# Optimization experiments

Hardware: AMD Instinct MI355X
Metric: run time of the kernel (lower is better)

Reference implementation:

```python
import jax, jax.numpy as jnp
import numpy as np
from jax import lax

T, B, I, H, FC, O = 2048, 64, 128, 128, 32, 2

def _xavier(key, shape):
    # torch xavier_normal_ on [..., fan_out, fan_in]
    std = float(np.sqrt(2.0 / (shape[-2] + shape[-1])))
    return jax.random.normal(key, shape, jnp.float32) * std

def setup_inputs() -> dict:
    key = jax.random.key(0)
    ks = jax.random.split(key, 16)
    inp = {
        'x': jax.random.normal(ks[0], (T, B, I), jnp.float32),
        'w_ig': _xavier(ks[1], (B, H, I)),
        'w_ii': _xavier(ks[2], (B, H, I)),
        'w_if': _xavier(ks[3], (B, H, I)),
        'w_io': _xavier(ks[4], (B, H, I)),
        'w_hg': _xavier(ks[5], (B, H, H)),
        'w_hi': _xavier(ks[6], (B, H, H)),
        'w_hf': _xavier(ks[7], (B, H, H)),
        'w_ho': _xavier(ks[8], (B, H, H)),
        'b_g': jnp.zeros((B, H, 1), jnp.float32),
        'b_i': jnp.zeros((B, H, 1), jnp.float32),
        'b_f': jnp.zeros((B, H, 1), jnp.float32),
        'b_o': jnp.zeros((B, H, 1), jnp.float32),
        'fc1_w': _xavier(ks[9], (FC, H)),
        'fc1_b': jnp.zeros((FC,), jnp.float32),
        'fc2_w': _xavier(ks[10], (O, FC)),
        'fc2_b': jnp.zeros((O,), jnp.float32),
    }
    return inp

def reference(x, w_ig, w_ii, w_if, w_io, w_hg, w_hi, w_hf, w_ho,
              b_g, b_i, b_f, b_o, fc1_w, fc1_b, fc2_w, fc2_b):
    b, h = w_hg.shape[0], w_hg.shape[1]
    # Original bug: gates read self.hidd which is never updated -> stays zeros.
    hidd0 = jnp.zeros((b, h), x.dtype)
    # Recurrent contributions (identically zero, kept for faithfulness)
    rg = jnp.einsum('bhk,bk->bh', w_hg, hidd0)
    ri = jnp.einsum('bhk,bk->bh', w_hi, hidd0)
    rf = jnp.einsum('bhk,bk->bh', w_hf, hidd0)
    ro = jnp.einsum('bhk,bk->bh', w_ho, hidd0)
    # Input gate pre-activations for all timesteps in one einsum each: [T,B,H]
    g = jnp.tanh(jnp.einsum('bhi,tbi->tbh', w_ig, x) + rg + b_g[:, :, 0])
    i_ = jax.nn.sigmoid(jnp.einsum('bhi,tbi->tbh', w_ii, x) + ri + b_i[:, :, 0])
    f = jax.nn.sigmoid(jnp.einsum('bhi,tbi->tbh', w_if, x) + rf + b_f[:, :, 0])
    o = jax.nn.sigmoid(jnp.einsum('bhi,tbi->tbh', w_io, x) + ro + b_o[:, :, 0])

    def step(carry, gifo):
        c, _ = carry
        g_t, i_t, f_t, o_t = gifo
        c = f_t * c + i_t * g_t
        hid = o_t * jnp.tanh(c)
        return (c, hid), None

    c0 = jnp.zeros((b, h), x.dtype)
    (c_fin, h_fin), _ = lax.scan(step, (c0, c0), (g, i_, f, o))
    # classifier on last hidden: Linear -> tanh -> Linear -> log_softmax
    z = jnp.tanh(h_fin @ fc1_w.T + fc1_b) @ fc2_w.T + fc2_b
    return jax.nn.log_softmax(z, axis=1)
```

## Files before the change

kernel.cpp:

```cpp
#include <hip/hip_runtime.h>
#include <hip/hip_bf16.h>
#include <cstddef>

#define T_DIM 2048
#define B_DIM 64
#define I_DIM 128
#define H_DIM 128
#define FC_DIM 32
#define O_DIM 2

#define NC 16
#define TC (T_DIM / NC)
#define MT 8

#define LOG2E  1.44269504088896f
#define LOG2E2 2.88539008177793f

typedef __attribute__((ext_vector_type(8))) short bf16x8;
typedef __attribute__((ext_vector_type(4))) float f32x4;

__device__ __forceinline__ bf16x8 cvt8(const float* __restrict__ p) {
    union { bf16x8 v; __hip_bfloat162 h2[4]; } u;
#pragma unroll
    for (int j = 0; j < 4; ++j) {
        float2 f2 = {p[2 * j], p[2 * j + 1]};
        u.h2[j] = __float22bfloat162_rn(f2);
    }
    return u.v;
}

__global__ void convert_w_kernel(const float* __restrict__ wg,
                                 const float* __restrict__ wi,
                                 const float* __restrict__ wf,
                                 short* __restrict__ og,
                                 short* __restrict__ oi,
                                 short* __restrict__ of)
{
    const float* src = (blockIdx.y == 0) ? wg : (blockIdx.y == 1) ? wi : wf;
    short* dst       = (blockIdx.y == 0) ? og : (blockIdx.y == 1) ? oi : of;
    const float scale = (blockIdx.y == 0) ? LOG2E2 : LOG2E;
    const size_t idx = ((size_t)blockIdx.x * 256 + threadIdx.x) * 8;
    float4 u0 = *(const float4*)(src + idx);
    float4 u1 = *(const float4*)(src + idx + 4);
    float a[8] = {u0.x * scale, u0.y * scale, u0.z * scale, u0.w * scale,
                  u1.x * scale, u1.y * scale, u1.z * scale, u1.w * scale};
    *(bf16x8*)(dst + idx) = cvt8(a);
}

__global__ __launch_bounds__(512, 4)
void gates_scan_kernel(const float* __restrict__ x,
    const short* __restrict__ wg, const short* __restrict__ wi,
    const short* __restrict__ wf,
    const float* __restrict__ b_g, const float* __restrict__ b_i,
    const float* __restrict__ b_f,
    float* __restrict__ wsF, float* __restrict__ wsA)
{
    __shared__ short frag[MT * 4 * 64 * 8];

    const int L    = threadIdx.x & 63;
    const int wv   = threadIdx.x >> 6;
    const int col  = L & 15;
    const int quad = L >> 4;
    const int bid  = blockIdx.x;
    const int b     = bid & (B_DIM - 1);
    const int chunk = bid >> 6;

    const int h = wv * 16 + col;
    bf16x8 Bg[4], Bi[4], Bf[4];
    {
        const size_t wo = ((size_t)b * H_DIM + h) * I_DIM + quad * 8;
#pragma unroll
        for (int kk = 0; kk < 4; ++kk) {
            Bg[kk] = *(const bf16x8*)(wg + wo + kk * 32);
            Bi[kk] = *(const bf16x8*)(wi + wo + kk * 32);
            Bf[kk] = *(const bf16x8*)(wf + wo + kk * 32);
        }
    }
    const float biasg = b_g[b * H_DIM + h] * LOG2E2;
    const float biasi = b_i[b * H_DIM + h] * LOG2E;
    const float biasf = b_f[b * H_DIM + h] * LOG2E;

    {
        const int mt = wv;
        const int tl = (col >> 2) * 32 + mt * 4 + (col & 3);
        const float* xp = x + ((size_t)(chunk * TC + tl) * B_DIM + b) * I_DIM;
#pragma unroll
        for (int kk = 0; kk < 4; ++kk) {
            const int i0 = quad * 8 + kk * 32;
            float4 u0 = *(const float4*)(xp + i0);
            float4 u1 = *(const float4*)(xp + i0 + 4);
            float a[8] = {u0.x, u0.y, u0.z, u0.w, u1.x, u1.y, u1.z, u1.w};
            *(bf16x8*)(frag + (((mt * 4 + kk) * 64) + L) * 8) = cvt8(a);
        }
    }
    __syncthreads();

    float Fq = 1.0f, Aq = 0.0f;
#pragma unroll 2
    for (int mt = 0; mt < MT; ++mt) {
        bf16x8 ah[4];
#pragma unroll
        for (int kk = 0; kk < 4; ++kk)
            ah[kk] = *(const bf16x8*)(frag + (((mt * 4 + kk) * 64) + L) * 8);
        f32x4 accg = {0.f, 0.f, 0.f, 0.f};
        f32x4 acci = {0.f, 0.f, 0.f, 0.f};
        f32x4 accf = {0.f, 0.f, 0.f, 0.f};
#pragma unroll
        for (int kk = 0; kk < 4; ++kk) {
            accg = __builtin_amdgcn_mfma_f32_16x16x32_bf16(ah[kk], Bg[kk], accg, 0, 0, 0);
            acci = __builtin_amdgcn_mfma_f32_16x16x32_bf16(ah[kk], Bi[kk], acci, 0, 0, 0);
            accf = __builtin_amdgcn_mfma_f32_16x16x32_bf16(ah[kk], Bf[kk], accf, 0, 0, 0);
        }
#pragma unroll
        for (int r = 0; r < 4; ++r) {
            float g  = 2.0f * __builtin_amdgcn_rcpf(
                           1.0f + __builtin_amdgcn_exp2f(-(accg[r] + biasg))) - 1.0f;
            float iv = __builtin_amdgcn_rcpf(
                           1.0f + __builtin_amdgcn_exp2f(-(acci[r] + biasi)));
            float fv = __builtin_amdgcn_rcpf(
                           1.0f + __builtin_amdgcn_exp2f(-(accf[r] + biasf)));
            Aq = fv * Aq + iv * g;
            Fq = fv * Fq;
        }
    }

    float Fo = __shfl_xor(Fq, 16, 64);
    float Ao = __shfl_xor(Aq, 16, 64);
    if ((quad & 1) == 0) { Aq = Fo * Aq + Ao; Fq = Fo * Fq; }
    else                 { Aq = Fq * Ao + Aq; Fq = Fq * Fo; }
    Fo = __shfl_xor(Fq, 32, 64);
    Ao = __shfl_xor(Aq, 32, 64);
    if (quad < 2) { Aq = Fo * Aq + Ao; Fq = Fo * Fq; }
    else          { Aq = Fq * Ao + Aq; Fq = Fq * Fo; }

    if (quad == 0) {
        const int idx = (b * NC + chunk) * H_DIM + h;
        wsF[idx] = Fq;
        wsA[idx] = Aq;
    }
}

__global__ void finish_kernel(const float* __restrict__ x,
    const float* __restrict__ w_io, const float* __restrict__ b_o,
    const float* __restrict__ fc1_w, const float* __restrict__ fc1_b,
    const float* __restrict__ fc2_w, const float* __restrict__ fc2_b,
    const float* __restrict__ wsF, const float* __restrict__ wsA,
    float* __restrict__ out)
{
    const int b = blockIdx.x;
    const int h = threadIdx.x;
    __shared__ float hf[H_DIM];
    __shared__ float z1[FC_DIM];

    float c = 0.0f;
#pragma unroll
    for (int nc = 0; nc < NC; ++nc) {
        const int idx = (b * NC + nc) * H_DIM + h;
        c = wsF[idx] * c + wsA[idx];
    }
    const float* xl = x + ((size_t)(T_DIM - 1) * B_DIM + b) * I_DIM;
    const float* wo = w_io + ((size_t)b * H_DIM + h) * I_DIM;
    float acc = b_o[b * H_DIM + h];
#pragma unroll 8
    for (int i = 0; i < I_DIM; i += 4) {
        float4 xa = *(const float4*)(xl + i);
        float4 wa = *(const float4*)(wo + i);
        acc += xa.x * wa.x + xa.y * wa.y + xa.z * wa.z + xa.w * wa.w;
    }
    const float o = 1.0f / (1.0f + expf(-acc));
    hf[h] = o * tanhf(c);
    __syncthreads();

    if (h < FC_DIM) {
        float a = fc1_b[h];
        const float* w1 = fc1_w + h * H_DIM;
        for (int i = 0; i < H_DIM; ++i) a += w1[i] * hf[i];
        z1[h] = tanhf(a);
    }
    __syncthreads();

    if (h == 0) {
        float z0 = fc2_b[0], zo1 = fc2_b[1];
        for (int j = 0; j < FC_DIM; ++j) {
            z0  += fc2_w[j] * z1[j];
            zo1 += fc2_w[FC_DIM + j] * z1[j];
        }
        const float m = fmaxf(z0, zo1);
        const float lse = m + logf(expf(z0 - m) + expf(zo1 - m));
        out[b * O_DIM + 0] = z0 - lse;
        out[b * O_DIM + 1] = zo1 - lse;
    }
}

extern "C" void kernel_launch(void* const* d_in, const int* in_sizes, int n_in,
                              void* d_out, int out_size, void* d_ws, size_t ws_size,
                              hipStream_t stream) {
    const float* x     = (const float*)d_in[0];
    const float* w_ig  = (const float*)d_in[1];
    const float* w_ii  = (const float*)d_in[2];
    const float* w_if  = (const float*)d_in[3];
    const float* w_io  = (const float*)d_in[4];
    const float* b_g   = (const float*)d_in[9];
    const float* b_i   = (const float*)d_in[10];
    const float* b_f   = (const float*)d_in[11];
    const float* b_o   = (const float*)d_in[12];
    const float* fc1_w = (const float*)d_in[13];
    const float* fc1_b = (const float*)d_in[14];
    const float* fc2_w = (const float*)d_in[15];
    const float* fc2_b = (const float*)d_in[16];

    const size_t NW = (size_t)B_DIM * H_DIM * I_DIM;
    short* wgc = (short*)d_ws;
    short* wic = wgc + NW;
    short* wfc = wic + NW;
    float* wsF = (float*)(wfc + NW);
    float* wsA = wsF + (size_t)B_DIM * NC * H_DIM;
    float* out = (float*)d_out;

    convert_w_kernel<<<dim3(NW / (256 * 8), 3), 256, 0, stream>>>(
        w_ig, w_ii, w_if, wgc, wic, wfc);

    gates_scan_kernel<<<dim3(B_DIM * NC), 512, 0, stream>>>(
        x, wgc, wic, wfc, b_g, b_i, b_f, wsF, wsA);

    finish_kernel<<<B_DIM, 128, 0, stream>>>(x, w_io, b_o, fc1_w, fc1_b,
                                             fc2_w, fc2_b, wsF, wsA, out);
}
```

Before: 157.1 us.

## Process two time chunks per block with register-prefetched next chunk of x

Each gates-scan block now handles two consecutive time chunks, so the per-block bf16 weight fragments are loaded once and reused across both chunks. While the current chunk runs its MFMA and gate math, the next chunk's x is prefetched into registers and converted into shared memory afterwards. This halves the grid to 512 blocks, which cuts weight reload traffic but lowers parallelism and adds register pressure plus extra barriers.

```diff
diff --git a/kernel.cpp b/kernel.cpp
--- a/kernel.cpp
+++ b/kernel.cpp
@@ -12,6 +12,7 @@
 #define NC 16
 #define TC (T_DIM / NC)
 #define MT 8
+#define CPB 2
 
 #define LOG2E  1.44269504088896f
 #define LOG2E2 2.88539008177793f
@@ -62,8 +63,8 @@
     const int col  = L & 15;
     const int quad = L >> 4;
     const int bid  = blockIdx.x;
-    const int b     = bid & (B_DIM - 1);
-    const int chunk = bid >> 6;
+    const int b    = bid & (B_DIM - 1);
+    const int cp   = bid >> 6;
 
     const int h = wv * 16 + col;
     bf16x8 Bg[4], Bi[4], Bf[4];
@@ -80,63 +81,93 @@
     const float biasi = b_i[b * H_DIM + h] * LOG2E;
     const float biasf = b_f[b * H_DIM + h] * LOG2E;
 
+    const int tl = (col >> 2) * 32 + wv * 4 + (col & 3);
+
     {
-        const int mt = wv;
-        const int tl = (col >> 2) * 32 + mt * 4 + (col & 3);
-        const float* xp = x + ((size_t)(chunk * TC + tl) * B_DIM + b) * I_DIM;
+        const float* xp = x + ((size_t)(cp * CPB * TC + tl) * B_DIM + b) * I_DIM;
 #pragma unroll
         for (int kk = 0; kk < 4; ++kk) {
             const int i0 = quad * 8 + kk * 32;
             float4 u0 = *(const float4*)(xp + i0);
             float4 u1 = *(const float4*)(xp + i0 + 4);
             float a[8] = {u0.x, u0.y, u0.z, u0.w, u1.x, u1.y, u1.z, u1.w};
-            *(bf16x8*)(frag + (((mt * 4 + kk) * 64) + L) * 8) = cvt8(a);
+            *(bf16x8*)(frag + (((wv * 4 + kk) * 64) + L) * 8) = cvt8(a);
         }
     }
     __syncthreads();
 
-    float Fq = 1.0f, Aq = 0.0f;
+    float4 px[8];
+
+#pragma unroll
+    for (int j = 0; j < CPB; ++j) {
+        const int c = cp * CPB + j;
+
+        if (j + 1 < CPB) {
+            const float* xp = x + ((size_t)((c + 1) * TC + tl) * B_DIM + b) * I_DIM;
+#pragma unroll
+            for (int kk = 0; kk < 4; ++kk) {
+                const int i0 = quad * 8 + kk * 32;
+                px[2 * kk]     = *(const float4*)(xp + i0);
+                px[2 * kk + 1] = *(const float4*)(xp + i0 + 4);
+            }
+        }
+
+        float Fq = 1.0f, Aq = 0.0f;
 #pragma unroll 2
-    for (int mt = 0; mt < MT; ++mt) {
-        bf16x8 ah[4];
-#pragma unroll
-        for (int kk = 0; kk < 4; ++kk)
-            ah[kk] = *(const bf16x8*)(frag + (((mt * 4 + kk) * 64) + L) * 8);
-        f32x4 accg = {0.f, 0.f, 0.f, 0.f};
-        f32x4 acci = {0.f, 0.f, 0.f, 0.f};
-        f32x4 accf = {0.f, 0.f, 0.f, 0.f};
-#pragma unroll
-        for (int kk = 0; kk < 4; ++kk) {
-            accg = __builtin_amdgcn_mfma_f32_16x16x32_bf16(ah[kk], Bg[kk], accg, 0, 0, 0);
-            acci = __builtin_amdgcn_mfma_f32_16x16x32_bf16(ah[kk], Bi[kk], acci, 0, 0, 0);
-            accf = __builtin_amdgcn_mfma_f32_16x16x32_bf16(ah[kk], Bf[kk], accf, 0, 0, 0);
-        }
-#pragma unroll
-        for (int r = 0; r < 4; ++r) {
-            float g  = 2.0f * __builtin_amdgcn_rcpf(
-                           1.0f + __builtin_amdgcn_exp2f(-(accg[r] + biasg))) - 1.0f;
-            float iv = __builtin_amdgcn_rcpf(
-                           1.0f + __builtin_amdgcn_exp2f(-(acci[r] + biasi)));
-            float fv = __builtin_amdgcn_rcpf(
-                           1.0f + __builtin_amdgcn_exp2f(-(accf[r] + biasf)));
-            Aq = fv * Aq + iv * g;
-            Fq = fv * Fq;
-        }
-    }
-
-    float Fo = __shfl_xor(Fq, 16, 64);
-    float Ao = __shfl_xor(Aq, 16, 64);
-    if ((quad & 1) == 0) { Aq = Fo * Aq + Ao; Fq = Fo * Fq; }
-    else                 { Aq = Fq * Ao + Aq; Fq = Fq * Fo; }
-    Fo = __shfl_xor(Fq, 32, 64);
-    Ao = __shfl_xor(Aq, 32, 64);
-    if (quad < 2) { Aq = Fo * Aq + Ao; Fq = Fo * Fq; }
-    else          { Aq = Fq * Ao + Aq; Fq = Fq * Fo; }
-
-    if (quad == 0) {
-        const int idx = (b * NC + chunk) * H_DIM + h;
-        wsF[idx] = Fq;
-        wsA[idx] = Aq;
+        for (int mt = 0; mt < MT; ++mt) {
+            bf16x8 ah[4];
+#pragma unroll
+            for (int kk = 0; kk < 4; ++kk)
+                ah[kk] = *(const bf16x8*)(frag + (((mt * 4 + kk) * 64) + L) * 8);
+            f32x4 accg = {0.f, 0.f, 0.f, 0.f};
+            f32x4 acci = {0.f, 0.f, 0.f, 0.f};
+            f32x4 accf = {0.f, 0.f, 0.f, 0.f};
+#pragma unroll
+            for (int kk = 0; kk < 4; ++kk) {
+                accg = __builtin_amdgcn_mfma_f32_16x16x32_bf16(ah[kk], Bg[kk], accg, 0, 0, 0);
+                acci = __builtin_amdgcn_mfma_f32_16x16x32_bf16(ah[kk], Bi[kk], acci, 0, 0, 0);
+                accf = __builtin_amdgcn_mfma_f32_16x16x32_bf16(ah[kk], Bf[kk], accf, 0, 0, 0);
+            }
+#pragma unroll
+            for (int r = 0; r < 4; ++r) {
+                float g  = 2.0f * __builtin_amdgcn_rcpf(
+                               1.0f + __builtin_amdgcn_exp2f(-(accg[r] + biasg))) - 1.0f;
+                float iv = __builtin_amdgcn_rcpf(
+                               1.0f + __builtin_amdgcn_exp2f(-(acci[r] + biasi)));
+                float fv = __builtin_amdgcn_rcpf(
+                               1.0f + __builtin_amdgcn_exp2f(-(accf[r] + biasf)));
+                Aq = fv * Aq + iv * g;
+                Fq = fv * Fq;
+            }
+        }
+
+        float Fo = __shfl_xor(Fq, 16, 64);
+        float Ao = __shfl_xor(Aq, 16, 64);
+        if ((quad & 1) == 0) { Aq = Fo * Aq + Ao; Fq = Fo * Fq; }
+        else                 { Aq = Fq * Ao + Aq; Fq = Fq * Fo; }
+        Fo = __shfl_xor(Fq, 32, 64);
+        Ao = __shfl_xor(Aq, 32, 64);
+        if (quad < 2) { Aq = Fo * Aq + Ao; Fq = Fo * Fq; }
+        else          { Aq = Fq * Ao + Aq; Fq = Fq * Fo; }
+
+        if (quad == 0) {
+            const int idx = (b * NC + c) * H_DIM + h;
+            wsF[idx] = Fq;
+            wsA[idx] = Aq;
+        }
+
+        if (j + 1 < CPB) {
+            __syncthreads();
+#pragma unroll
+            for (int kk = 0; kk < 4; ++kk) {
+                float a[8] = {px[2 * kk].x,     px[2 * kk].y,
+                              px[2 * kk].z,     px[2 * kk].w,
+                              px[2 * kk + 1].x, px[2 * kk + 1].y,
+                              px[2 * kk + 1].z, px[2 * kk + 1].w};
+                *(bf16x8*)(frag + (((wv * 4 + kk) * 64) + L) * 8) = cvt8(a);
+            }
+            __syncthreads();
+        }
     }
 }
 
@@ -220,7 +251,7 @@
     convert_w_kernel<<<dim3(NW / (256 * 8), 3), 256, 0, stream>>>(
         w_ig, w_ii, w_if, wgc, wic, wfc);
 
-    gates_scan_kernel<<<dim3(B_DIM * NC), 512, 0, stream>>>(
+    gates_scan_kernel<<<dim3(B_DIM * NC / CPB), 512, 0, stream>>>(
         x, wgc, wic, wfc, b_g, b_i, b_f, wsF, wsA);
 
     finish_kernel<<<B_DIM, 128, 0, stream>>>(x, w_io, b_o, fc1_w, fc1_b,
```

Measured after the change: 160.4 us. +2.1%, slower.
